# Kernel optimization log

Hardware: AMD Instinct MI355X
Metric: run time of the kernel (lower is better)

## Reference

```python
import jax, jax.numpy as jnp
import numpy as np

BETA = 0.25
EPS = 1e-10


def setup_inputs() -> dict:
    key = jax.random.key(0)
    k1, k2 = jax.random.split(key)
    z = jax.random.normal(k1, (16, 256, 32, 32), dtype=jnp.float32)
    # Original init: uniform(-1/n_embed, 1/n_embed)
    n_embed, embed_dim = 8192, 256
    codebook = jax.random.uniform(k2, (n_embed, embed_dim), dtype=jnp.float32,
                                  minval=-1.0 / n_embed, maxval=1.0 / n_embed)
    return {"z": z, "codebook": codebook}


def reference(z, codebook):
    B, C, H, W = z.shape
    n_embed = codebook.shape[0]
    zp = jnp.transpose(z, (0, 2, 3, 1))            # (B,H,W,C)
    zf = zp.reshape(-1, C)                          # (N,C)
    # squared L2 distances (N, n_embed)
    d = (jnp.sum(zf * zf, axis=1, keepdims=True)
         + jnp.sum(codebook * codebook, axis=1)
         - 2.0 * zf @ codebook.T)
    idx = jnp.argmin(d, axis=1)                     # (N,)
    zq = codebook[idx].reshape(zp.shape)            # gather == one-hot @ codebook
    commitment_loss = jnp.mean((jax.lax.stop_gradient(zq) - zp) ** 2)
    embedding_loss = jnp.mean((zq - jax.lax.stop_gradient(zp)) ** 2)
    loss = embedding_loss + BETA * commitment_loss
    # straight-through estimator
    zq_st = zp + jax.lax.stop_gradient(zq - zp)
    # perplexity from mean one-hot usage (counts / N)
    counts = jnp.zeros((n_embed,), dtype=zf.dtype).at[idx].add(1.0)
    avg_probs = counts / zf.shape[0]
    perplexity = jnp.exp(-jnp.sum(avg_probs * jnp.log(avg_probs + EPS)))
    zq_out = jnp.transpose(zq_st, (0, 3, 1, 2))     # (B,C,H,W)
    return zq_out, loss, perplexity, idx
```

## Files before the change

### kernel.cpp

```cpp
#include <hip/hip_runtime.h>
#include <math.h>

#define Nrows 16384
#define NE 8192
#define Kdim 256
#define HWsz 1024
#define NSPL 4
#define BETAF 0.25f
#define NGATHBLK 1024

typedef __attribute__((ext_vector_type(8))) short bf16x8;
typedef __attribute__((ext_vector_type(16))) float f32x16;
typedef unsigned short u16;

__device__ inline u16 bf16_rne(float x) {
  unsigned int u = __float_as_uint(x);
  return (u16)((u + 0x7FFFu + ((u >> 16) & 1u)) >> 16);
}
__device__ inline float bf16_tof(u16 h) {
  return __uint_as_float(((unsigned int)h) << 16);
}
__device__ inline void gll16(const void* g, void* l) {
  __builtin_amdgcn_global_load_lds(
      (const __attribute__((address_space(1))) unsigned int*)g,
      (__attribute__((address_space(3))) unsigned int*)l, 16, 0, 0);
}

__global__ __launch_bounds__(256) void cc_kernel(const float* __restrict__ cb,
                                                 float* __restrict__ cc) {
  int wave = threadIdx.x >> 6;
  int lane = threadIdx.x & 63;
  int row = blockIdx.x * 4 + wave;
  const float4 v = *(const float4*)(cb + (size_t)row * Kdim + lane * 4);
  float s = v.x * v.x + v.y * v.y + v.z * v.z + v.w * v.w;
  for (int off = 32; off; off >>= 1) s += __shfl_down(s, off);
  if (lane == 0) cc[row] = s;
}

__global__ __launch_bounds__(256) void conv_cb(const float* __restrict__ cb,
                                               u16* __restrict__ Cf) {
  const int g = blockIdx.x * 256 + threadIdx.x;
  const int j = g >> 4, k16 = g & 15;
  const float* src = cb + (size_t)j * Kdim + k16 * 16;
  float f[16];
#pragma unroll
  for (int q = 0; q < 4; ++q) {
    const float4 v = ((const float4*)src)[q];
    f[q * 4 + 0] = v.x; f[q * 4 + 1] = v.y; f[q * 4 + 2] = v.z; f[q * 4 + 3] = v.w;
  }
  u16 h[3][16];
#pragma unroll
  for (int i = 0; i < 16; ++i) {
    const u16 q0 = bf16_rne(f[i]);
    const float r1 = f[i] - bf16_tof(q0);
    const u16 q1 = bf16_rne(r1);
    const float r2 = r1 - bf16_tof(q1);
    h[0][i] = q0; h[1][i] = q1; h[2][i] = bf16_rne(r2);
  }
  const int j32 = j >> 5, li = j & 31;
#pragma unroll
  for (int arr = 0; arr < 3; ++arr) {
#pragma unroll
    for (int kh = 0; kh < 2; ++kh) {
      const size_t off = ((size_t)(j32 * 3 + arr) * 16 + k16) * 512 + (kh * 32 + li) * 8;
      *(int4*)(Cf + off) = *(int4*)&h[arr][kh * 8];
    }
  }
}

__global__ __launch_bounds__(256) void conv_z(const float* __restrict__ z,
                                              u16* __restrict__ Zf,
                                              float* __restrict__ zz) {
  __shared__ float tile[64][68];
  const int t = threadIdx.x;
  const int bid = blockIdx.x;
  const int n0 = bid * 64;
  const int b = bid >> 4;
  const int hw0 = (bid & 15) << 6;
  const float* zb = z + (size_t)b * (Kdim * HWsz) + hw0;
  float zzacc = 0.f;
  const int rr = t >> 2;
  const int kq = (t & 3) * 16;
  for (int kc = 0; kc < 4; ++kc) {
#pragma unroll
    for (int i = 0; i < 16; ++i) {
      const int idx = i * 256 + t;
      const int k = idx >> 6, r = idx & 63;
      tile[r][k] = zb[(size_t)(kc * 64 + k) * HWsz + r];
    }
    __syncthreads();
    if (t < 64) {
      for (int k = 0; k < 64; ++k) {
        const float a = tile[t][k];
        zzacc = fmaf(a, a, zzacc);
      }
    }
    u16 h[3][16];
#pragma unroll
    for (int i = 0; i < 16; ++i) {
      const float fv = tile[rr][kq + i];
      const u16 q0 = bf16_rne(fv);
      const float r1 = fv - bf16_tof(q0);
      const u16 q1 = bf16_rne(r1);
      const float r2 = r1 - bf16_tof(q1);
      h[0][i] = q0; h[1][i] = q1; h[2][i] = bf16_rne(r2);
    }
    const int k16 = kc * 4 + (t & 3);
    const int n32 = bid * 2 + (rr >> 5), li = rr & 31;
#pragma unroll
    for (int arr = 0; arr < 3; ++arr) {
#pragma unroll
      for (int kh = 0; kh < 2; ++kh) {
        const size_t off = ((size_t)(n32 * 3 + arr) * 16 + k16) * 512 + (kh * 32 + li) * 8;
        *(int4*)(Zf + off) = *(int4*)&h[arr][kh * 8];
      }
    }
    __syncthreads();
  }
  if (t < 64) zz[n0 + t] = zzacc;
}

__global__ __launch_bounds__(256, 2) void vq_gemm(
    const u16* __restrict__ Cf, const u16* __restrict__ Zf,
    const float* __restrict__ cc, const float* __restrict__ zz,
    float* __restrict__ pd, int* __restrict__ pj) {
  __shared__ __align__(16) u16 Al[4][3][3072];
  __shared__ float ccs[2048];

  const int t = threadIdx.x;
  const int lane = t & 63;
  const int w = __builtin_amdgcn_readfirstlane(t >> 6);
  const int bid = blockIdx.x;
  const int cg = bid & 3;
  const int rt = bid >> 2;
  const int n32 = rt * 4 + w;

#pragma unroll
  for (int i = 0; i < 8; ++i) ccs[i * 256 + t] = cc[cg * 2048 + i * 256 + t];

  const float zzv = zz[n32 * 32 + (lane & 31)];

  bf16x8 B[16][3];
#pragma unroll
  for (int kc = 0; kc < 16; ++kc)
#pragma unroll
    for (int arr = 0; arr < 3; ++arr)
      B[kc][arr] = *(const bf16x8*)(
          Zf + ((size_t)(n32 * 3 + arr) * 16 + kc) * 512 + lane * 8);

  u16* Aw = &Al[w][0][0];

#define STAGE(P, SL)                                                          \
  {                                                                           \
    const int pp_ = (P);                                                      \
    const int gg_ = pp_ >> 4;                                                 \
    const int ggc_ = gg_ < 32 ? gg_ : 0;                                      \
    const int kc_ = pp_ & 15;                                                 \
    _Pragma("unroll")                                                         \
    for (int i = 0; i < 6; ++i) {                                             \
      const int jx = i / 3, arr = i % 3;                                      \
      gll16(Cf + ((size_t)((cg * 64 + ggc_ * 2 + jx) * 3 + arr) * 16 + kc_)   \
                    * 512 + lane * 8,                                         \
            Aw + (SL) * 3072 + i * 512);                                      \
    }                                                                         \
  }

#define MF(af, bv, ac) ac = __builtin_amdgcn_mfma_f32_32x32x16_bf16(af, bv, ac, 0, 0, 0);
#define CHUNK(kcv)                                                            \
  {                                                                           \
    const u16* Ab = Aw + sl * 3072;                                           \
    bf16x8 a0[3], a1[3];                                                      \
    _Pragma("unroll")                                                         \
    for (int arr = 0; arr < 3; ++arr) {                                       \
      a0[arr] = *(const bf16x8*)(Ab + arr * 512 + lane * 8);                  \
      a1[arr] = *(const bf16x8*)(Ab + (3 + arr) * 512 + lane * 8);            \
    }                                                                         \
    MF(a0[0], B[kcv][0], acc0) MF(a1[0], B[kcv][0], acc1)                     \
    MF(a0[0], B[kcv][1], acc0) MF(a1[0], B[kcv][1], acc1)                     \
    MF(a0[1], B[kcv][0], acc0) MF(a1[1], B[kcv][0], acc1)                     \
    MF(a0[1], B[kcv][1], acc0) MF(a1[1], B[kcv][1], acc1)                     \
    MF(a0[0], B[kcv][2], acc0) MF(a1[0], B[kcv][2], acc1)                     \
    MF(a0[2], B[kcv][0], acc0) MF(a1[2], B[kcv][0], acc1)                     \
  }

#define ROT() { sl = (sl == 2) ? 0 : sl + 1; s2 = (s2 == 2) ? 0 : s2 + 1; }

  STAGE(0, 0)
  STAGE(1, 1)
  __syncthreads();

  float bd = INFINITY;
  int bj = 0;
  const f32x16 zero16 = {0,0,0,0,0,0,0,0,0,0,0,0,0,0,0,0};
  int sl = 0, s2 = 2;

  for (int g = 0; g < 32; ++g) {
    f32x16 acc0 = zero16, acc1 = zero16;
#pragma unroll
    for (int kc = 0; kc < 16; ++kc) {
      __builtin_amdgcn_sched_barrier(0);
      STAGE(g * 16 + kc + 2, s2)
      asm volatile("s_waitcnt vmcnt(12)" ::: "memory");
      __builtin_amdgcn_sched_barrier(0);
      CHUNK(kc)
      ROT()
    }

#pragma unroll
    for (int jx = 0; jx < 2; ++jx) {
      const f32x16& a = jx ? acc1 : acc0;
#pragma unroll
      for (int q = 0; q < 4; ++q) {
        const float4 c4 = *(const float4*)&ccs[g * 64 + jx * 32 + q * 8 + (lane >> 5) * 4];
        const float cv[4] = {c4.x, c4.y, c4.z, c4.w};
#pragma unroll
        for (int r = 0; r < 4; ++r) {
          const float d = (zzv + cv[r]) - 2.0f * a[q * 4 + r];
          const int j = cg * 2048 + g * 64 + jx * 32 + r + q * 8 + (lane >> 5) * 4;
          if (d < bd) { bd = d; bj = j; }
        }
      }
    }
  }
  asm volatile("s_waitcnt vmcnt(0)" ::: "memory");
#undef STAGE
#undef CHUNK
#undef MF
#undef ROT

  {
    const float od = __shfl_xor(bd, 32);
    const int oj = __shfl_xor(bj, 32);
    if (od < bd || (od == bd && oj < bj)) { bd = od; bj = oj; }
  }
  if (lane < 32) {
    const int n = n32 * 32 + lane;
    pd[(size_t)cg * Nrows + n] = bd;
    pj[(size_t)cg * Nrows + n] = bj;
  }
}

__global__ __launch_bounds__(256) void vq_gather_loss(
    const float* __restrict__ z, const float* __restrict__ cb,
    const float* __restrict__ pd, const int* __restrict__ pj,
    float* __restrict__ outz, float* __restrict__ out_idxf,
    int* __restrict__ counts, float* __restrict__ loss_part) {
  __shared__ float cbl[64 * 65];
  __shared__ int jr[64];
  __shared__ float ws4[4];
  const int t = threadIdx.x;
  const int bid = blockIdx.x;
  const int nt = bid >> 2;
  const int cq = bid & 3;
  const int b = nt >> 4;
  const int hw0 = (nt & 15) << 6;
  const int n0 = b * HWsz + hw0;

  if (t < 64) {
    const int n = n0 + t;
    float d0 = pd[n];
    int j0 = pj[n];
    for (int s = 1; s < NSPL; ++s) {
      const float d = pd[(size_t)s * Nrows + n];
      const int j = pj[(size_t)s * Nrows + n];
      if (d < d0 || (d == d0 && j < j0)) { d0 = d; j0 = j; }
    }
    jr[t] = j0;
    if (cq == 0) {
      out_idxf[n] = (float)j0;
      atomicAdd(&counts[j0], 1);
    }
  }
  __syncthreads();

  {
    const int r = t >> 2;
    const int c0 = (t & 3) * 16;
    const int j = jr[r];
    const float* src = cb + (size_t)j * Kdim + cq * 64 + c0;
#pragma unroll
    for (int q = 0; q < 4; ++q) {
      const float4 v = ((const float4*)src)[q];
      float* dst = &cbl[r * 65 + c0 + q * 4];
      dst[0] = v.x; dst[1] = v.y; dst[2] = v.z; dst[3] = v.w;
    }
  }
  __syncthreads();

  const int w = t >> 6, lane = t & 63;

  float ls = 0.f;
  for (int k = 0; k < 16; ++k) {
    const int cl = w * 16 + k;
    const int c = cq * 64 + cl;
    const float q = cbl[lane * 65 + cl];
    const size_t gidx = ((size_t)(b * Kdim + c)) * HWsz + hw0 + lane;
    const float zv = z[gidx];
    outz[gidx] = q;
    const float dd = q - zv;
    ls = fmaf(dd, dd, ls);
  }
  for (int off = 32; off; off >>= 1) ls += __shfl_down(ls, off);
  if (lane == 0) ws4[w] = ls;
  __syncthreads();
  if (t == 0) loss_part[bid] = (ws4[0] + ws4[1]) + (ws4[2] + ws4[3]);
}

__global__ __launch_bounds__(256) void vq_final(const int* __restrict__ counts,
                                                const float* __restrict__ loss_part,
                                                float* __restrict__ out_sc) {
  float h = 0.f;
  for (int i = threadIdx.x; i < NE; i += 256) {
    float p = (float)counts[i] * (1.0f / 16384.0f);
    h += p * logf(p + 1e-10f);
  }
  float ls = 0.f;
  for (int i = threadIdx.x; i < NGATHBLK; i += 256) ls += loss_part[i];
  for (int off = 32; off; off >>= 1) {
    h += __shfl_down(h, off);
    ls += __shfl_down(ls, off);
  }
  __shared__ float hs[4], lss[4];
  if ((threadIdx.x & 63) == 0) {
    hs[threadIdx.x >> 6] = h;
    lss[threadIdx.x >> 6] = ls;
  }
  __syncthreads();
  if (threadIdx.x == 0) {
    float H = (hs[0] + hs[1]) + (hs[2] + hs[3]);
    float L = (lss[0] + lss[1]) + (lss[2] + lss[3]);
    float m = L * (1.0f / 4194304.0f);
    out_sc[0] = m + BETAF * m;
    out_sc[1] = expf(-H);
  }
}

extern "C" void kernel_launch(void* const* d_in, const int* in_sizes, int n_in,
                              void* d_out, int out_size, void* d_ws, size_t ws_size,
                              hipStream_t stream) {
  const float* z = (const float*)d_in[0];
  const float* cb = (const float*)d_in[1];
  float* out = (float*)d_out;
  float* out_zq = out;
  float* out_sc = out + 4194304;
  float* out_idx = out + 4194306;

  char* wp = (char*)d_ws;
  u16* Cf = (u16*)wp;           wp += (size_t)NE * Kdim * 2 * 3;
  u16* Zf = (u16*)wp;           wp += (size_t)Nrows * Kdim * 2 * 3;
  float* cc = (float*)wp;       wp += (size_t)NE * 4;
  float* zz = (float*)wp;       wp += (size_t)Nrows * 4;
  float* pd = (float*)wp;       wp += (size_t)NSPL * Nrows * 4;
  int* pj = (int*)wp;           wp += (size_t)NSPL * Nrows * 4;
  int* counts = (int*)wp;       wp += (size_t)NE * 4;
  float* loss_part = (float*)wp; wp += (size_t)NGATHBLK * 4;

  hipMemsetAsync(counts, 0, (size_t)NE * 4, stream);

  cc_kernel<<<NE / 4, 256, 0, stream>>>(cb, cc);
  conv_cb<<<NE * 16 / 256, 256, 0, stream>>>(cb, Cf);
  conv_z<<<Nrows / 64, 256, 0, stream>>>(z, Zf, zz);
  vq_gemm<<<512, 256, 0, stream>>>(Cf, Zf, cc, zz, pd, pj);
  vq_gather_loss<<<NGATHBLK, 256, 0, stream>>>(z, cb, pd, pj, out_zq, out_idx,
                                               counts, loss_part);
  vq_final<<<1, 256, 0, stream>>>(counts, loss_part, out_sc);
}
```

Before: 500.7 us.

## Load codebook fragments directly into registers with double buffering instead of LDS staging

Replaces the per-wave LDS triple-buffer, filled by global_load_lds, with direct global-to-register loads of the codebook MFMA fragments. Two register sets alternate so the next chunk's loads are issued while the current chunk's MFMAs run. This removes the LDS round-trip and the explicit vmcnt/sched_barrier pipeline and frees the LDS. In exchange it raises VGPR pressure, which can threaten the 2-blocks-per-CU occupancy, and it leaves load/compute overlap to the compiler's waitcnt placement.

```diff
diff --git a/kernel.cpp b/kernel.cpp
--- a/kernel.cpp
+++ b/kernel.cpp
@@ -19,11 +19,6 @@
 }
 __device__ inline float bf16_tof(u16 h) {
   return __uint_as_float(((unsigned int)h) << 16);
-}
-__device__ inline void gll16(const void* g, void* l) {
-  __builtin_amdgcn_global_load_lds(
-      (const __attribute__((address_space(1))) unsigned int*)g,
-      (__attribute__((address_space(3))) unsigned int*)l, 16, 0, 0);
 }
 
 __global__ __launch_bounds__(256) void cc_kernel(const float* __restrict__ cb,
@@ -124,7 +119,6 @@
     const u16* __restrict__ Cf, const u16* __restrict__ Zf,
     const float* __restrict__ cc, const float* __restrict__ zz,
     float* __restrict__ pd, int* __restrict__ pj) {
-  __shared__ __align__(16) u16 Al[4][3][3072];
   __shared__ float ccs[2048];
 
   const int t = threadIdx.x;
@@ -148,62 +142,47 @@
       B[kc][arr] = *(const bf16x8*)(
           Zf + ((size_t)(n32 * 3 + arr) * 16 + kc) * 512 + lane * 8);
 
-  u16* Aw = &Al[w][0][0];
-
-#define STAGE(P, SL)                                                          \
-  {                                                                           \
-    const int pp_ = (P);                                                      \
-    const int gg_ = pp_ >> 4;                                                 \
-    const int ggc_ = gg_ < 32 ? gg_ : 0;                                      \
-    const int kc_ = pp_ & 15;                                                 \
-    _Pragma("unroll")                                                         \
-    for (int i = 0; i < 6; ++i) {                                             \
-      const int jx = i / 3, arr = i % 3;                                      \
-      gll16(Cf + ((size_t)((cg * 64 + ggc_ * 2 + jx) * 3 + arr) * 16 + kc_)   \
-                    * 512 + lane * 8,                                         \
-            Aw + (SL) * 3072 + i * 512);                                      \
-    }                                                                         \
-  }
+  __syncthreads();
+
+#define ALD(dst, gg, kcv, i_)                                                 \
+  dst = *(const bf16x8*)(Cf +                                                 \
+      (((size_t)(cg * 64 + (gg) * 2 + ((i_) / 3)) * 3 + ((i_) % 3)) * 16 +    \
+       (kcv)) * 512 + lane * 8);
 
 #define MF(af, bv, ac) ac = __builtin_amdgcn_mfma_f32_32x32x16_bf16(af, bv, ac, 0, 0, 0);
-#define CHUNK(kcv)                                                            \
-  {                                                                           \
-    const u16* Ab = Aw + sl * 3072;                                           \
-    bf16x8 a0[3], a1[3];                                                      \
-    _Pragma("unroll")                                                         \
-    for (int arr = 0; arr < 3; ++arr) {                                       \
-      a0[arr] = *(const bf16x8*)(Ab + arr * 512 + lane * 8);                  \
-      a1[arr] = *(const bf16x8*)(Ab + (3 + arr) * 512 + lane * 8);            \
-    }                                                                         \
-    MF(a0[0], B[kcv][0], acc0) MF(a1[0], B[kcv][0], acc1)                     \
-    MF(a0[0], B[kcv][1], acc0) MF(a1[0], B[kcv][1], acc1)                     \
-    MF(a0[1], B[kcv][0], acc0) MF(a1[1], B[kcv][0], acc1)                     \
-    MF(a0[1], B[kcv][1], acc0) MF(a1[1], B[kcv][1], acc1)                     \
-    MF(a0[0], B[kcv][2], acc0) MF(a1[0], B[kcv][2], acc1)                     \
-    MF(a0[2], B[kcv][0], acc0) MF(a1[2], B[kcv][0], acc1)                     \
-  }
-
-#define ROT() { sl = (sl == 2) ? 0 : sl + 1; s2 = (s2 == 2) ? 0 : s2 + 1; }
-
-  STAGE(0, 0)
-  STAGE(1, 1)
-  __syncthreads();
+#define MFSET(bk, kcv)                                                        \
+  MF(bk[0], B[kcv][0], acc0) MF(bk[3], B[kcv][0], acc1)                       \
+  MF(bk[0], B[kcv][1], acc0) MF(bk[3], B[kcv][1], acc1)                       \
+  MF(bk[1], B[kcv][0], acc0) MF(bk[4], B[kcv][0], acc1)                       \
+  MF(bk[1], B[kcv][1], acc0) MF(bk[4], B[kcv][1], acc1)                       \
+  MF(bk[0], B[kcv][2], acc0) MF(bk[3], B[kcv][2], acc1)                       \
+  MF(bk[2], B[kcv][0], acc0) MF(bk[5], B[kcv][0], acc1)
 
   float bd = INFINITY;
   int bj = 0;
   const f32x16 zero16 = {0,0,0,0,0,0,0,0,0,0,0,0,0,0,0,0};
-  int sl = 0, s2 = 2;
+
+  bf16x8 Ae[6], Ao[6];
+
+#pragma unroll
+  for (int i = 0; i < 6; ++i) { ALD(Ae[i], 0, 0, i) }
 
   for (int g = 0; g < 32; ++g) {
     f32x16 acc0 = zero16, acc1 = zero16;
 #pragma unroll
     for (int kc = 0; kc < 16; ++kc) {
-      __builtin_amdgcn_sched_barrier(0);
-      STAGE(g * 16 + kc + 2, s2)
-      asm volatile("s_waitcnt vmcnt(12)" ::: "memory");
-      __builtin_amdgcn_sched_barrier(0);
-      CHUNK(kc)
-      ROT()
+      const int P = g * 16 + kc + 1;
+      const int gn = (P >> 4) < 32 ? (P >> 4) : 0;
+      const int kn = P & 15;
+      if ((kc & 1) == 0) {
+#pragma unroll
+        for (int i = 0; i < 6; ++i) { ALD(Ao[i], gn, kn, i) }
+        MFSET(Ae, kc)
+      } else {
+#pragma unroll
+        for (int i = 0; i < 6; ++i) { ALD(Ae[i], gn, kn, i) }
+        MFSET(Ao, kc)
+      }
     }
 
 #pragma unroll
@@ -222,11 +201,9 @@
       }
     }
   }
-  asm volatile("s_waitcnt vmcnt(0)" ::: "memory");
-#undef STAGE
-#undef CHUNK
+#undef ALD
 #undef MF
-#undef ROT
+#undef MFSET
 
   {
     const float od = __shfl_xor(bd, 32);
```

Measured after the change: 588.5 us. 17.6% more time.
